# Optimization experiments

Measured on AMD Instinct MI355X. Metric: run time of the kernel, lower is better.

The kernel has to match this reference:

```python
import jax, jax.numpy as jnp
import numpy as np

HIDDEN = 2048
HEADS = 16
HEAD_DIM = HIDDEN // HEADS  # 128


def setup_inputs() -> dict:
    key = jax.random.key(0)
    ks = jax.random.split(key, 9)
    B, S = 2, 2048
    x = jax.random.normal(ks[0], (B, S, HIDDEN), dtype=jnp.float32)
    scale = 1.0 / np.sqrt(HIDDEN)
    Wq = jax.random.normal(ks[1], (HIDDEN, HIDDEN), dtype=jnp.float32) * scale
    Wk = jax.random.normal(ks[2], (HIDDEN, HIDDEN), dtype=jnp.float32) * scale
    Wv = jax.random.normal(ks[3], (HIDDEN, HIDDEN), dtype=jnp.float32) * scale
    Wo = jax.random.normal(ks[4], (HIDDEN, HIDDEN), dtype=jnp.float32) * scale
    bq = jnp.zeros((HIDDEN,), dtype=jnp.float32)
    bk = jnp.zeros((HIDDEN,), dtype=jnp.float32)
    bv = jnp.zeros((HIDDEN,), dtype=jnp.float32)
    bo = jnp.zeros((HIDDEN,), dtype=jnp.float32)
    return {"x": x, "Wq": Wq, "bq": bq, "Wk": Wk, "bk": bk,
            "Wv": Wv, "bv": bv, "Wo": Wo, "bo": bo}


def reference(x, Wq, bq, Wk, bk, Wv, bv, Wo, bo):
    B, S, H = x.shape
    nh, hd = HEADS, HEAD_DIM
    # projections: Linear stores W as [out, in], applies x @ W.T + b
    q = (x @ Wq.T + bq).reshape(B, S, nh, hd).transpose(0, 2, 1, 3)  # [B,nh,S,hd]
    k = (x @ Wk.T + bk).reshape(B, S, nh, hd).transpose(0, 2, 1, 3)
    v = (x @ Wv.T + bv).reshape(B, S, nh, hd).transpose(0, 2, 1, 3)
    scores = jnp.einsum("bhqd,bhkd->bhqk", q, k) / np.sqrt(hd)  # [B,nh,S,S]
    causal = jnp.tril(jnp.ones((S, S), dtype=bool))
    scores = jnp.where(causal[None, None], scores, -jnp.inf)
    probs = jax.nn.softmax(scores, axis=-1)
    attn = jnp.einsum("bhqk,bhkd->bhqd", probs, v)  # [B,nh,S,hd]
    y = attn.transpose(0, 2, 1, 3).reshape(B, S, H)
    return y @ Wo.T + bo
```

## Files before the change

### kernel.cpp

```cpp
#include <hip/hip_runtime.h>
#include <hip/hip_bf16.h>

#define HIDDEN 2048
#define NH 16
#define HD 128
#define BATCH 2
#define SEQ 2048

typedef __attribute__((ext_vector_type(8))) short short8;
typedef __attribute__((ext_vector_type(4))) float floatx4;

__device__ inline unsigned short f2bf(float f) {
  union { float f; unsigned int u; } x; x.f = f;
  unsigned int r = x.u + 0x7fffu + ((x.u >> 16) & 1u);
  return (unsigned short)(r >> 16);
}

__device__ inline void async_cp16(const void* g, void* l) {
  __builtin_amdgcn_global_load_lds(
      (const __attribute__((address_space(1))) unsigned int*)g,
      (__attribute__((address_space(3))) unsigned int*)l, 16, 0, 0);
}

__global__ __launch_bounds__(256) void cvt_kernel(const float* __restrict__ in,
                                                  unsigned short* __restrict__ out,
                                                  int n) {
  int i = (blockIdx.x * 256 + threadIdx.x) * 4;
  if (i + 3 < n) {
    float4 v = *reinterpret_cast<const float4*>(in + i);
    ushort4 o;
    o.x = f2bf(v.x); o.y = f2bf(v.y); o.z = f2bf(v.z); o.w = f2bf(v.w);
    *reinterpret_cast<ushort4*>(out + i) = o;
  }
}

template<int MODE>
__global__ __launch_bounds__(256, 2) void gemm_nt(const unsigned short* __restrict__ A,
                                                  const unsigned short* __restrict__ Bw,
                                                  const float* __restrict__ bias,
                                                  float* __restrict__ outF,
                                                  unsigned short* __restrict__ outQ) {
  __shared__ __align__(16) unsigned short As[4][128][8];
  __shared__ __align__(16) unsigned short Bs[4][128][8];
  const int t = threadIdx.x;
  const int lane = t & 63;
  const int w = t >> 6;
  const int wr = w >> 1, wc = w & 1;
  const int row0 = blockIdx.x * 128;
  const int col0 = blockIdx.y * 128;

  floatx4 acc[4][4] = {};

  for (int kt = 0; kt < 2048 / 32; ++kt) {
    __syncthreads();
    const int kb = kt * 32;
#pragma unroll
    for (int cc = 0; cc < 2; ++cc) {
      int c = t + cc * 256;
      int k8 = c >> 7;
      int r = c & 127;
      async_cp16(A + (size_t)(row0 + r) * 2048 + kb + k8 * 8, &As[0][0][0] + c * 8);
      async_cp16(Bw + (size_t)(col0 + r) * 2048 + kb + k8 * 8, &Bs[0][0][0] + c * 8);
    }
    __syncthreads();

    short8 af[4], bf[4];
#pragma unroll
    for (int m = 0; m < 4; ++m)
      af[m] = *(const short8*)&As[lane >> 4][wr * 64 + m * 16 + (lane & 15)][0];
#pragma unroll
    for (int n = 0; n < 4; ++n)
      bf[n] = *(const short8*)&Bs[lane >> 4][wc * 64 + n * 16 + (lane & 15)][0];
#pragma unroll
    for (int m = 0; m < 4; ++m)
#pragma unroll
      for (int n = 0; n < 4; ++n)
        acc[m][n] = __builtin_amdgcn_mfma_f32_16x16x32_bf16(af[m], bf[n], acc[m][n], 0, 0, 0);
  }

#pragma unroll
  for (int m = 0; m < 4; ++m) {
#pragma unroll
    for (int n = 0; n < 4; ++n) {
      int gcol = col0 + wc * 64 + n * 16 + (lane & 15);
      float bv = bias[gcol];
#pragma unroll
      for (int r = 0; r < 4; ++r) {
        int grow = row0 + wr * 64 + m * 16 + (lane >> 4) * 4 + r;
        float v = acc[m][n][r] + bv;
        if (MODE == 1) {
          outF[(size_t)grow * 2048 + gcol] = v;
        } else {
          int bb = grow >> 11;
          int ss = grow & 2047;
          int hh = gcol >> 7;
          int dd = gcol & 127;
          outQ[(((size_t)bb * NH + hh) * SEQ + ss) * HD + dd] = f2bf(v);
        }
      }
    }
  }
}

__global__ __launch_bounds__(256, 2) void attn_kernel(const unsigned short* __restrict__ Q,
                                                      const unsigned short* __restrict__ Kg,
                                                      const unsigned short* __restrict__ Vg,
                                                      unsigned short* __restrict__ O) {
  __shared__ __align__(16) unsigned short Ks[16][32][8];
  __shared__ __align__(16) unsigned short VT[4096];
  __shared__ __align__(16) unsigned short Ps[4][512];

  const int t = threadIdx.x;
  const int lane = t & 63;
  const int w = t >> 6;
  const int bh = blockIdx.y;
  const int q0 = blockIdx.x * 64;
  const int bb = bh >> 4;
  const int hh = bh & 15;

  const unsigned short* Qb = Q + (size_t)bh * SEQ * HD;
  const unsigned short* Kb = Kg + (size_t)bh * SEQ * HD;
  const unsigned short* Vb = Vg + (size_t)bh * SEQ * HD;

  const int qw = q0 + w * 16;
  short8 aq[4];
#pragma unroll
  for (int kb = 0; kb < 4; ++kb)
    aq[kb] = *(const short8*)(Qb + (size_t)(qw + (lane & 15)) * HD + kb * 32 + (lane >> 4) * 8);

  floatx4 acc[8] = {};
  float mrun[4], lrun[4];
#pragma unroll
  for (int r = 0; r < 4; ++r) { mrun[r] = -1e30f; lrun[r] = 0.f; }

  const float scale = 0.08838834764831845f;
  const int ntiles = (q0 >> 5) + 2;

  for (int tk = 0; tk < ntiles; ++tk) {
    const int k0 = tk * 32;
    __syncthreads();
#pragma unroll
    for (int cc = 0; cc < 2; ++cc) {
      int c = t + cc * 256;
      async_cp16(Kb + (size_t)(k0 + (c & 31)) * HD + (c >> 5) * 8, &Ks[0][0][0] + c * 8);
    }
#pragma unroll
    for (int cc = 0; cc < 2; ++cc) {
      int c = t + cc * 256;
      int kv = c >> 4;
      int d0 = (c & 15) * 8;
      short8 vv = *(const short8*)(Vb + (size_t)(k0 + kv) * HD + d0);
#pragma unroll
      for (int j = 0; j < 8; ++j) {
        int dd = d0 + j;
        VT[((kv >> 3) * 1024) + ((dd ^ ((dd >> 3) & 7)) * 8) + (kv & 7)] = (unsigned short)vv[j];
      }
    }
    __syncthreads();

    float sv[2][4];
#pragma unroll
    for (int nb = 0; nb < 2; ++nb) {
      floatx4 s = {0.f, 0.f, 0.f, 0.f};
#pragma unroll
      for (int kb = 0; kb < 4; ++kb) {
        short8 bk = *(const short8*)&Ks[kb * 4 + (lane >> 4)][nb * 16 + (lane & 15)][0];
        s = __builtin_amdgcn_mfma_f32_16x16x32_bf16(aq[kb], bk, s, 0, 0, 0);
      }
#pragma unroll
      for (int r = 0; r < 4; ++r) sv[nb][r] = s[r] * scale;
    }
    if (k0 + 31 > q0) {
#pragma unroll
      for (int nb = 0; nb < 2; ++nb) {
        int kvg = k0 + nb * 16 + (lane & 15);
#pragma unroll
        for (int r = 0; r < 4; ++r) {
          int qg = qw + (lane >> 4) * 4 + r;
          if (kvg > qg) sv[nb][r] = -1e30f;
        }
      }
    }
#pragma unroll
    for (int r = 0; r < 4; ++r) {
      float mx = fmaxf(sv[0][r], sv[1][r]);
#pragma unroll
      for (int off = 8; off >= 1; off >>= 1)
        mx = fmaxf(mx, __shfl_xor(mx, off, 64));
      float mnew = fmaxf(mrun[r], mx);
      float p0 = __expf(sv[0][r] - mnew);
      float p1 = __expf(sv[1][r] - mnew);
      sv[0][r] = p0; sv[1][r] = p1;
      float rs = p0 + p1;
#pragma unroll
      for (int off = 8; off >= 1; off >>= 1)
        rs += __shfl_xor(rs, off, 64);
      float f = __expf(mrun[r] - mnew);
      lrun[r] = lrun[r] * f + rs;
      mrun[r] = mnew;
#pragma unroll
      for (int db = 0; db < 8; ++db) acc[db][r] *= f;
    }
    unsigned short* ps = &Ps[w][0];
#pragma unroll
    for (int nb = 0; nb < 2; ++nb)
#pragma unroll
      for (int r = 0; r < 4; ++r)
        ps[((nb * 2 + ((lane & 15) >> 3)) * 16 + (lane >> 4) * 4 + r) * 8 + (lane & 7)] =
            f2bf(sv[nb][r]);
    short8 pa = *(const short8*)(ps + (lane >> 4) * 128 + (lane & 15) * 8);
#pragma unroll
    for (int db = 0; db < 8; ++db) {
      int dg = db * 16 + (lane & 15);
      short8 bv = *(const short8*)&VT[((lane >> 4) * 1024) + ((dg ^ ((dg >> 3) & 7)) * 8)];
      acc[db] = __builtin_amdgcn_mfma_f32_16x16x32_bf16(pa, bv, acc[db], 0, 0, 0);
    }
  }

#pragma unroll
  for (int r = 0; r < 4; ++r) {
    float inv = 1.0f / lrun[r];
    int qg = qw + (lane >> 4) * 4 + r;
#pragma unroll
    for (int db = 0; db < 8; ++db) {
      int dg = hh * HD + db * 16 + (lane & 15);
      O[((size_t)bb * SEQ + qg) * HIDDEN + dg] = f2bf(acc[db][r] * inv);
    }
  }
}

extern "C" void kernel_launch(void* const* d_in, const int* in_sizes, int n_in,
                              void* d_out, int out_size, void* d_ws, size_t ws_size,
                              hipStream_t stream) {
  (void)in_sizes; (void)n_in; (void)out_size; (void)ws_size;
  const float* x  = (const float*)d_in[0];
  const float* Wq = (const float*)d_in[1];
  const float* bq = (const float*)d_in[2];
  const float* Wk = (const float*)d_in[3];
  const float* bk = (const float*)d_in[4];
  const float* Wv = (const float*)d_in[5];
  const float* bv = (const float*)d_in[6];
  const float* Wo = (const float*)d_in[7];
  const float* bo = (const float*)d_in[8];
  float* out = (float*)d_out;

  char* ws = (char*)d_ws;
  unsigned short* xbf = (unsigned short*)ws;
  unsigned short* Wbf = (unsigned short*)(ws + 16777216);
  unsigned short* Qbf = (unsigned short*)(ws + 25165824);
  unsigned short* Kbf = (unsigned short*)(ws + 41943040);
  unsigned short* Vbf = (unsigned short*)(ws + 58720256);

  dim3 blk(256);
  dim3 gg(32, 16);
  dim3 ga(32, 32);

  cvt_kernel<<<8192, blk, 0, stream>>>(x, xbf, BATCH * SEQ * HIDDEN);

  cvt_kernel<<<4096, blk, 0, stream>>>(Wq, Wbf, HIDDEN * HIDDEN);
  gemm_nt<0><<<gg, blk, 0, stream>>>(xbf, Wbf, bq, nullptr, Qbf);

  cvt_kernel<<<4096, blk, 0, stream>>>(Wk, Wbf, HIDDEN * HIDDEN);
  gemm_nt<0><<<gg, blk, 0, stream>>>(xbf, Wbf, bk, nullptr, Kbf);

  cvt_kernel<<<4096, blk, 0, stream>>>(Wv, Wbf, HIDDEN * HIDDEN);
  gemm_nt<0><<<gg, blk, 0, stream>>>(xbf, Wbf, bv, nullptr, Vbf);

  attn_kernel<<<ga, blk, 0, stream>>>(Qbf, Kbf, Vbf, xbf);

  cvt_kernel<<<4096, blk, 0, stream>>>(Wo, Wbf, HIDDEN * HIDDEN);
  gemm_nt<1><<<gg, blk, 0, stream>>>(xbf, Wbf, bo, out, nullptr);
}
```

Baseline: 648.4 us.

## Double-buffer GEMM loads and retile attention to 128-query blocks with transposed scores

The GEMM now double-buffers its LDS tiles, prefetching the next K slice with async copies while the current one is multiplied, which cuts one barrier per iteration. The attention kernel is restructured: each block handles 128 queries (32 per wave) against 64-key tiles. It computes S^T so probabilities stay in registers and are packed straight into MFMA operands, with no LDS round trip. It also uses a packed, XOR-swizzled V transpose and a 1D grid that pairs heavy and light causal blocks for load balance. Dropping the occupancy hint and holding more accumulators raises register pressure.

```diff
diff --git a/kernel.cpp b/kernel.cpp
--- a/kernel.cpp
+++ b/kernel.cpp
@@ -1,5 +1,4 @@
 #include <hip/hip_runtime.h>
-#include <hip/hip_bf16.h>
 
 #define HIDDEN 2048
 #define NH 16
@@ -14,6 +13,9 @@
   union { float f; unsigned int u; } x; x.f = f;
   unsigned int r = x.u + 0x7fffu + ((x.u >> 16) & 1u);
   return (unsigned short)(r >> 16);
+}
+__device__ inline unsigned int pkbf(float a, float b) {
+  return (unsigned int)f2bf(a) | ((unsigned int)f2bf(b) << 16);
 }
 
 __device__ inline void async_cp16(const void* g, void* l) {
@@ -35,13 +37,13 @@
 }
 
 template<int MODE>
-__global__ __launch_bounds__(256, 2) void gemm_nt(const unsigned short* __restrict__ A,
-                                                  const unsigned short* __restrict__ Bw,
-                                                  const float* __restrict__ bias,
-                                                  float* __restrict__ outF,
-                                                  unsigned short* __restrict__ outQ) {
-  __shared__ __align__(16) unsigned short As[4][128][8];
-  __shared__ __align__(16) unsigned short Bs[4][128][8];
+__global__ __launch_bounds__(256) void gemm_nt(const unsigned short* __restrict__ A,
+                                               const unsigned short* __restrict__ Bw,
+                                               const float* __restrict__ bias,
+                                               float* __restrict__ outF,
+                                               unsigned short* __restrict__ outQ) {
+  __shared__ __align__(16) unsigned short As[2][4096];
+  __shared__ __align__(16) unsigned short Bs[2][4096];
   const int t = threadIdx.x;
   const int lane = t & 63;
   const int w = t >> 6;
@@ -51,31 +53,41 @@
 
   floatx4 acc[4][4] = {};
 
-  for (int kt = 0; kt < 2048 / 32; ++kt) {
-    __syncthreads();
-    const int kb = kt * 32;
-#pragma unroll
-    for (int cc = 0; cc < 2; ++cc) {
-      int c = t + cc * 256;
-      int k8 = c >> 7;
-      int r = c & 127;
-      async_cp16(A + (size_t)(row0 + r) * 2048 + kb + k8 * 8, &As[0][0][0] + c * 8);
-      async_cp16(Bw + (size_t)(col0 + r) * 2048 + kb + k8 * 8, &Bs[0][0][0] + c * 8);
-    }
-    __syncthreads();
-
+#pragma unroll
+  for (int cc = 0; cc < 2; ++cc) {
+    int c = t + cc * 256;
+    int k8 = c >> 7, r = c & 127;
+    async_cp16(A + (size_t)(row0 + r) * 2048 + k8 * 8, &As[0][c * 8]);
+    async_cp16(Bw + (size_t)(col0 + r) * 2048 + k8 * 8, &Bs[0][c * 8]);
+  }
+  __syncthreads();
+
+  int buf = 0;
+  for (int kt = 0; kt < 64; ++kt) {
+    if (kt < 63) {
+      const int kb = (kt + 1) * 32;
+#pragma unroll
+      for (int cc = 0; cc < 2; ++cc) {
+        int c = t + cc * 256;
+        int k8 = c >> 7, r = c & 127;
+        async_cp16(A + (size_t)(row0 + r) * 2048 + kb + k8 * 8, &As[buf ^ 1][c * 8]);
+        async_cp16(Bw + (size_t)(col0 + r) * 2048 + kb + k8 * 8, &Bs[buf ^ 1][c * 8]);
+      }
+    }
     short8 af[4], bf[4];
 #pragma unroll
     for (int m = 0; m < 4; ++m)
-      af[m] = *(const short8*)&As[lane >> 4][wr * 64 + m * 16 + (lane & 15)][0];
+      af[m] = *(const short8*)&As[buf][(lane >> 4) * 1024 + (wr * 64 + m * 16 + (lane & 15)) * 8];
 #pragma unroll
     for (int n = 0; n < 4; ++n)
-      bf[n] = *(const short8*)&Bs[lane >> 4][wc * 64 + n * 16 + (lane & 15)][0];
+      bf[n] = *(const short8*)&Bs[buf][(lane >> 4) * 1024 + (wc * 64 + n * 16 + (lane & 15)) * 8];
 #pragma unroll
     for (int m = 0; m < 4; ++m)
 #pragma unroll
       for (int n = 0; n < 4; ++n)
         acc[m][n] = __builtin_amdgcn_mfma_f32_16x16x32_bf16(af[m], bf[n], acc[m][n], 0, 0, 0);
+    __syncthreads();
+    buf ^= 1;
   }
 
 #pragma unroll
@@ -102,19 +114,24 @@
   }
 }
 
-__global__ __launch_bounds__(256, 2) void attn_kernel(const unsigned short* __restrict__ Q,
-                                                      const unsigned short* __restrict__ Kg,
-                                                      const unsigned short* __restrict__ Vg,
-                                                      unsigned short* __restrict__ O) {
-  __shared__ __align__(16) unsigned short Ks[16][32][8];
-  __shared__ __align__(16) unsigned short VT[4096];
-  __shared__ __align__(16) unsigned short Ps[4][512];
+__global__ __launch_bounds__(256) void attn_kernel(const unsigned short* __restrict__ Q,
+                                                   const unsigned short* __restrict__ Kg,
+                                                   const unsigned short* __restrict__ Vg,
+                                                   unsigned short* __restrict__ O) {
+  __shared__ __align__(16) unsigned short Ks[16 * 64 * 8];
+  __shared__ __align__(16) unsigned short VT[8 * 128 * 8];
 
   const int t = threadIdx.x;
   const int lane = t & 63;
   const int w = t >> 6;
-  const int bh = blockIdx.y;
-  const int q0 = blockIdx.x * 64;
+  const int g = lane >> 4;
+  const int l15 = lane & 15;
+
+  int gid = blockIdx.x;
+  int Wi = (gid < 256) ? gid : 767 - gid;
+  const int bx = Wi & 15;
+  const int bh = Wi >> 4;
+  const int q0 = bx * 128;
   const int bb = bh >> 4;
   const int hh = bh & 15;
 
@@ -122,109 +139,151 @@
   const unsigned short* Kb = Kg + (size_t)bh * SEQ * HD;
   const unsigned short* Vb = Vg + (size_t)bh * SEQ * HD;
 
-  const int qw = q0 + w * 16;
-  short8 aq[4];
-#pragma unroll
-  for (int kb = 0; kb < 4; ++kb)
-    aq[kb] = *(const short8*)(Qb + (size_t)(qw + (lane & 15)) * HD + kb * 32 + (lane >> 4) * 8);
-
-  floatx4 acc[8] = {};
-  float mrun[4], lrun[4];
-#pragma unroll
-  for (int r = 0; r < 4; ++r) { mrun[r] = -1e30f; lrun[r] = 0.f; }
-
+  const int qw = q0 + w * 32;
+
+  short8 bq[2][4];
+#pragma unroll
+  for (int qh = 0; qh < 2; ++qh)
+#pragma unroll
+    for (int kb = 0; kb < 4; ++kb)
+      bq[qh][kb] = *(const short8*)(Qb + (size_t)(qw + qh * 16 + l15) * HD + kb * 32 + g * 8);
+
+  floatx4 acc[2][8] = {};
+  float mrun[2] = {-1e30f, -1e30f};
+  float lrun[2] = {0.f, 0.f};
   const float scale = 0.08838834764831845f;
-  const int ntiles = (q0 >> 5) + 2;
-
+
+  const int ntiles = (q0 >> 6) + 2;
   for (int tk = 0; tk < ntiles; ++tk) {
-    const int k0 = tk * 32;
+    const int k0 = tk * 64;
     __syncthreads();
+#pragma unroll
+    for (int cc = 0; cc < 4; ++cc) {
+      int c = t + cc * 256;
+      int k8 = c >> 6, s = c & 63;
+      int kvs = ((s >> 5) << 5) + (((s >> 2) & 3) << 3) + (((s >> 4) & 1) << 2) + (s & 3);
+      async_cp16(Kb + (size_t)(k0 + kvs) * HD + k8 * 8, &Ks[c * 8]);
+    }
 #pragma unroll
     for (int cc = 0; cc < 2; ++cc) {
       int c = t + cc * 256;
-      async_cp16(Kb + (size_t)(k0 + (c & 31)) * HD + (c >> 5) * 8, &Ks[0][0][0] + c * 8);
-    }
-#pragma unroll
-    for (int cc = 0; cc < 2; ++cc) {
-      int c = t + cc * 256;
-      int kv = c >> 4;
+      int kv = (c >> 4) * 2;
       int d0 = (c & 15) * 8;
-      short8 vv = *(const short8*)(Vb + (size_t)(k0 + kv) * HD + d0);
+      int row = kv >> 3;
+      short8 va = *(const short8*)(Vb + (size_t)(k0 + kv) * HD + d0);
+      short8 vb = *(const short8*)(Vb + (size_t)(k0 + kv + 1) * HD + d0);
 #pragma unroll
       for (int j = 0; j < 8; ++j) {
-        int dd = d0 + j;
-        VT[((kv >> 3) * 1024) + ((dd ^ ((dd >> 3) & 7)) * 8) + (kv & 7)] = (unsigned short)vv[j];
+        int d = d0 + j;
+        int dp = d ^ (((d >> 3) ^ row) & 7);
+        unsigned int u = (unsigned short)va[j] | ((unsigned int)(unsigned short)vb[j] << 16);
+        *(unsigned int*)&VT[(row * 128 + dp) * 8 + (kv & 7)] = u;
       }
     }
     __syncthreads();
 
-    float sv[2][4];
-#pragma unroll
-    for (int nb = 0; nb < 2; ++nb) {
-      floatx4 s = {0.f, 0.f, 0.f, 0.f};
+    floatx4 sv[4][2];
+#pragma unroll
+    for (int kvh = 0; kvh < 4; ++kvh) {
+      sv[kvh][0] = (floatx4){0.f, 0.f, 0.f, 0.f};
+      sv[kvh][1] = (floatx4){0.f, 0.f, 0.f, 0.f};
 #pragma unroll
       for (int kb = 0; kb < 4; ++kb) {
-        short8 bk = *(const short8*)&Ks[kb * 4 + (lane >> 4)][nb * 16 + (lane & 15)][0];
-        s = __builtin_amdgcn_mfma_f32_16x16x32_bf16(aq[kb], bk, s, 0, 0, 0);
-      }
-#pragma unroll
-      for (int r = 0; r < 4; ++r) sv[nb][r] = s[r] * scale;
-    }
-    if (k0 + 31 > q0) {
-#pragma unroll
-      for (int nb = 0; nb < 2; ++nb) {
-        int kvg = k0 + nb * 16 + (lane & 15);
+        short8 ak = *(const short8*)&Ks[((kb * 4 + g) * 64 + kvh * 16 + l15) * 8];
+        sv[kvh][0] = __builtin_amdgcn_mfma_f32_16x16x32_bf16(ak, bq[0][kb], sv[kvh][0], 0, 0, 0);
+        sv[kvh][1] = __builtin_amdgcn_mfma_f32_16x16x32_bf16(ak, bq[1][kb], sv[kvh][1], 0, 0, 0);
+      }
+    }
+
+    const bool domask = (k0 + 63 > qw);
+#pragma unroll
+    for (int kvh = 0; kvh < 4; ++kvh)
+#pragma unroll
+      for (int qh = 0; qh < 2; ++qh)
 #pragma unroll
         for (int r = 0; r < 4; ++r) {
-          int qg = qw + (lane >> 4) * 4 + r;
-          if (kvg > qg) sv[nb][r] = -1e30f;
+          float s = sv[kvh][qh][r] * scale;
+          if (domask) {
+            int kvg = k0 + ((kvh >> 1) << 5) + g * 8 + ((kvh & 1) << 2) + r;
+            int qg = qw + qh * 16 + l15;
+            if (kvg > qg) s = -1e30f;
+          }
+          sv[kvh][qh][r] = s;
         }
-      }
-    }
+
+#pragma unroll
+    for (int qh = 0; qh < 2; ++qh) {
+      float mt = sv[0][qh][0];
+#pragma unroll
+      for (int kvh = 0; kvh < 4; ++kvh)
+#pragma unroll
+        for (int r = 0; r < 4; ++r)
+          mt = fmaxf(mt, sv[kvh][qh][r]);
+      mt = fmaxf(mt, __shfl_xor(mt, 16, 64));
+      mt = fmaxf(mt, __shfl_xor(mt, 32, 64));
+      float mnew = fmaxf(mrun[qh], mt);
+      float f = __expf(mrun[qh] - mnew);
+      mrun[qh] = mnew;
+      float ssum = 0.f;
+#pragma unroll
+      for (int kvh = 0; kvh < 4; ++kvh)
+#pragma unroll
+        for (int r = 0; r < 4; ++r) {
+          float p = __expf(sv[kvh][qh][r] - mnew);
+          sv[kvh][qh][r] = p;
+          ssum += p;
+        }
+      ssum += __shfl_xor(ssum, 16, 64);
+      ssum += __shfl_xor(ssum, 32, 64);
+      lrun[qh] = lrun[qh] * f + ssum;
+      float fr[4];
+#pragma unroll
+      for (int r = 0; r < 4; ++r)
+        fr[r] = __shfl(f, (lane & 48) + 4 * (lane >> 4) + r, 64);
+#pragma unroll
+      for (int db = 0; db < 8; ++db)
+#pragma unroll
+        for (int r = 0; r < 4; ++r)
+          acc[qh][db][r] *= fr[r];
+    }
+
+#pragma unroll
+    for (int kh = 0; kh < 2; ++kh) {
+      union { short8 s8; unsigned int u[4]; } p0, p1;
+      p0.u[0] = pkbf(sv[2 * kh][0][0], sv[2 * kh][0][1]);
+      p0.u[1] = pkbf(sv[2 * kh][0][2], sv[2 * kh][0][3]);
+      p0.u[2] = pkbf(sv[2 * kh + 1][0][0], sv[2 * kh + 1][0][1]);
+      p0.u[3] = pkbf(sv[2 * kh + 1][0][2], sv[2 * kh + 1][0][3]);
+      p1.u[0] = pkbf(sv[2 * kh][1][0], sv[2 * kh][1][1]);
+      p1.u[1] = pkbf(sv[2 * kh][1][2], sv[2 * kh][1][3]);
+      p1.u[2] = pkbf(sv[2 * kh + 1][1][0], sv[2 * kh + 1][1][1]);
+      p1.u[3] = pkbf(sv[2 * kh + 1][1][2], sv[2 * kh + 1][1][3]);
+      int row = kh * 4 + g;
+#pragma unroll
+      for (int db = 0; db < 8; ++db) {
+        int d = db * 16 + l15;
+        int dp = d ^ (((d >> 3) ^ row) & 7);
+        short8 bv = *(const short8*)&VT[(row * 128 + dp) * 8];
+        acc[0][db] = __builtin_amdgcn_mfma_f32_16x16x32_bf16(p0.s8, bv, acc[0][db], 0, 0, 0);
+        acc[1][db] = __builtin_amdgcn_mfma_f32_16x16x32_bf16(p1.s8, bv, acc[1][db], 0, 0, 0);
+      }
+    }
+  }
+
+#pragma unroll
+  for (int qh = 0; qh < 2; ++qh) {
+    float inv = 1.0f / lrun[qh];
+    float ir[4];
+#pragma unroll
+    for (int r = 0; r < 4; ++r)
+      ir[r] = __shfl(inv, (lane & 48) + 4 * (lane >> 4) + r, 64);
 #pragma unroll
     for (int r = 0; r < 4; ++r) {
-      float mx = fmaxf(sv[0][r], sv[1][r]);
-#pragma unroll
-      for (int off = 8; off >= 1; off >>= 1)
-        mx = fmaxf(mx, __shfl_xor(mx, off, 64));
-      float mnew = fmaxf(mrun[r], mx);
-      float p0 = __expf(sv[0][r] - mnew);
-      float p1 = __expf(sv[1][r] - mnew);
-      sv[0][r] = p0; sv[1][r] = p1;
-      float rs = p0 + p1;
-#pragma unroll
-      for (int off = 8; off >= 1; off >>= 1)
-        rs += __shfl_xor(rs, off, 64);
-      float f = __expf(mrun[r] - mnew);
-      lrun[r] = lrun[r] * f + rs;
-      mrun[r] = mnew;
-#pragma unroll
-      for (int db = 0; db < 8; ++db) acc[db][r] *= f;
-    }
-    unsigned short* ps = &Ps[w][0];
-#pragma unroll
-    for (int nb = 0; nb < 2; ++nb)
-#pragma unroll
-      for (int r = 0; r < 4; ++r)
-        ps[((nb * 2 + ((lane & 15) >> 3)) * 16 + (lane >> 4) * 4 + r) * 8 + (lane & 7)] =
-            f2bf(sv[nb][r]);
-    short8 pa = *(const short8*)(ps + (lane >> 4) * 128 + (lane & 15) * 8);
-#pragma unroll
-    for (int db = 0; db < 8; ++db) {
-      int dg = db * 16 + (lane & 15);
-      short8 bv = *(const short8*)&VT[((lane >> 4) * 1024) + ((dg ^ ((dg >> 3) & 7)) * 8)];
-      acc[db] = __builtin_amdgcn_mfma_f32_16x16x32_bf16(pa, bv, acc[db], 0, 0, 0);
-    }
-  }
-
-#pragma unroll
-  for (int r = 0; r < 4; ++r) {
-    float inv = 1.0f / lrun[r];
-    int qg = qw + (lane >> 4) * 4 + r;
-#pragma unroll
-    for (int db = 0; db < 8; ++db) {
-      int dg = hh * HD + db * 16 + (lane & 15);
-      O[((size_t)bb * SEQ + qg) * HIDDEN + dg] = f2bf(acc[db][r] * inv);
+      int qg = qw + qh * 16 + 4 * g + r;
+      size_t base = ((size_t)bb * SEQ + qg) * HIDDEN + hh * HD;
+#pragma unroll
+      for (int db = 0; db < 8; ++db)
+        O[base + db * 16 + l15] = f2bf(acc[qh][db][r] * ir[r]);
     }
   }
 }
@@ -253,7 +312,7 @@
 
   dim3 blk(256);
   dim3 gg(32, 16);
-  dim3 ga(32, 32);
+  dim3 ga(512);
 
   cvt_kernel<<<8192, blk, 0, stream>>>(x, xbf, BATCH * SEQ * HIDDEN);
 
```

After: 615.1 us. 5.1% less time.
